# Optimization experiments

Hardware: AMD Instinct MI355X
Metric: run time of the kernel (lower is better)

The kernel has to match this reference:

```python
import jax, jax.numpy as jnp
import numpy as np

N_QUBITS = 8
N_LAYERS = 2


def _ry(theta):
    # theta: scalar or (B,) -> (...,2,2) complex64 RY matrix
    c = jnp.cos(theta * 0.5)
    s = jnp.sin(theta * 0.5)
    return jnp.stack([jnp.stack([c, -s], -1), jnp.stack([s, c], -1)], -2).astype(jnp.complex64)


def _rz(theta):
    # theta: scalar -> (2,2) complex64 RZ matrix diag(e^{-i t/2}, e^{i t/2})
    e = jnp.exp(-0.5j * theta.astype(jnp.complex64))
    z = jnp.zeros_like(e)
    return jnp.stack([jnp.stack([e, z], -1), jnp.stack([z, jnp.conj(e)], -1)], -2)


def _apply_1q(psi, U, wire):
    # U: (2,2) shared across batch; psi: (B, 2,2,...,2)
    ax = wire + 1
    psi = jnp.moveaxis(psi, ax, -1)
    psi = jnp.einsum('...i,ji->...j', psi, U)
    return jnp.moveaxis(psi, -1, ax)


def _apply_1q_batched(psi, U, wire):
    # U: (B,2,2) per-sample gate (angle embedding)
    ax = wire + 1
    psi = jnp.moveaxis(psi, ax, -1)
    psi = jnp.einsum('b...i,bji->b...j', psi, U)
    return jnp.moveaxis(psi, -1, ax)


def _apply_cnot(psi, ctrl, tgt):
    c_ax, t_ax = ctrl + 1, tgt + 1
    psi0 = jnp.take(psi, 0, axis=c_ax)
    psi1 = jnp.take(psi, 1, axis=c_ax)
    t2 = t_ax - 1 if t_ax > c_ax else t_ax
    psi1 = jnp.flip(psi1, axis=t2)  # X on target when control=1
    return jnp.stack([psi0, psi1], axis=c_ax)


def _circuit(x, weights):
    n = N_QUBITS
    B = x.shape[0]
    psi = jnp.zeros((B,) + (2,) * n, jnp.complex64)
    psi = psi.at[(slice(None),) + (0,) * n].set(1.0)
    ang = x * (np.pi / 2)
    for layer in range(weights.shape[0]):
        # AngleEmbedding: RY(x_i * pi/2) on each wire, per-sample angles
        for i in range(n):
            psi = _apply_1q_batched(psi, _ry(ang[:, i]), i)
        # trainable rotations
        for i in range(n):
            psi = _apply_1q(psi, _ry(weights[layer, i, 0]), i)
            psi = _apply_1q(psi, _rz(weights[layer, i, 1]), i)
        # CNOT ring
        for i in range(n - 1):
            psi = _apply_cnot(psi, i, i + 1)
        psi = _apply_cnot(psi, n - 1, 0)
    # <Z_i> = sum_s |psi_s|^2 * (+1 if bit_i(s)==0 else -1)
    p = (psi.real ** 2 + psi.imag ** 2).reshape(B, 2 ** n)
    bits = (jnp.arange(2 ** n)[:, None] >> (n - 1 - jnp.arange(n))) & 1
    zsign = (1 - 2 * bits).astype(jnp.float32)  # (256, 8)
    return (p @ zsign).astype(jnp.float32)


def setup_inputs() -> dict:
    key = jax.random.key(0)
    k1, k2 = jax.random.split(key)
    x = jax.random.uniform(k1, (65536, N_QUBITS), jnp.float32)
    weights = jax.random.uniform(k2, (N_LAYERS, N_QUBITS, 2), jnp.float32) * (2.0 * np.pi)
    return {"x": x, "weights": weights}


def reference(x, weights):
    return _circuit(x, weights)
```

## Files before the change

kernel.cpp:

```cpp
#include <hip/hip_runtime.h>

#define PI_OVER_2 1.57079632679489661923f


__global__ __launch_bounds__(256) void qpauli2_kernel(
        const float* __restrict__ x, const float* __restrict__ w,
        float* __restrict__ out, int nsamples) {
    const int sample = blockIdx.x * blockDim.x + threadIdx.x;
    if (sample >= nsamples) return;

    const float4* xv = reinterpret_cast<const float4*>(x + (size_t)sample * 8);
    const float4 xa = xv[0], xb = xv[1];
    const float xs[8] = {xa.x, xa.y, xa.z, xa.w, xb.x, xb.y, xb.z, xb.w};

    float C[8], S[8], zb[8], xbv[8], yb[8];
#pragma unroll
    for (int q = 0; q < 8; ++q) {
        const float A1 = fmaf(xs[q], PI_OVER_2, w[2 * q]);
        const float W  = w[2 * q + 1];
        const float A2 = fmaf(xs[q], PI_OVER_2, w[16 + 2 * q]);
        float s1v, c1v, sw, cw;
        __sincosf(A1, &s1v, &c1v);
        __sincosf(W, &sw, &cw);
        __sincosf(A2, &S[q], &C[q]);
        zb[q] = c1v;
        xbv[q] = s1v * cw;
        yb[q] = s1v * sw;
    }
    float ZT[9];
    ZT[8] = 1.f;
#pragma unroll
    for (int k = 7; k >= 2; --k) ZT[k] = zb[k] * ZT[k + 1];

    float o[8];

    float fre[16], fim[16];
#pragma unroll
    for (int i2 = 0; i2 < 16; ++i2) { fre[i2] = 0.f; fim[i2] = 0.f; }
    fre[2] = C[0];
    fre[6] = C[0] * zb[0];
    fre[1] = -S[0] * xbv[0];
    fim[5] = S[0] * yb[0];

#define FSTEP(Q)                                                              \
    {                                                                         \
        const float Cz = C[Q] * zb[Q], Cx = C[Q] * xbv[Q], Cy = C[Q] * yb[Q]; \
        const float Sz = S[Q] * zb[Q], Sx = S[Q] * xbv[Q], Sy = S[Q] * yb[Q]; \
        float nre[16], nim[16];                                               \
        _Pragma("unroll")                                                     \
        for (int i2 = 0; i2 < 16; ++i2) { nre[i2] = 0.f; nim[i2] = 0.f; }     \
        _Pragma("unroll")                                                     \
        for (int st = 0; st < 16; ++st) {                                     \
            const int dp_ = st & 1, z0 = (st >> 1) & 1;                       \
            const int H = (st >> 2) & 1, P = (st >> 3) & 1;                   \
            _Pragma("unroll")                                                 \
            for (int d = 0; d < 2; ++d) {                                     \
                const int mx = dp_ ^ d;                                       \
                const int mz = z0 ^ H ^ P;                                    \
                const int ns = d | (z0 << 1) | (H << 2) | ((P ^ d ^ 1) << 3); \
                if (mx == 0 && mz == 0) {                                     \
                    const float F = d ? -S[Q] : C[Q];                         \
                    nre[ns] = fmaf(F, fre[st], nre[ns]);                      \
                    nim[ns] = fmaf(F, fim[st], nim[ns]);                      \
                } else if (mx == 0 && mz == 1) {                              \
                    const float F = d ? -Sz : Cz;                             \
                    nre[ns] = fmaf(F, fre[st], nre[ns]);                      \
                    nim[ns] = fmaf(F, fim[st], nim[ns]);                      \
                } else if (mx == 1 && mz == 0) {                              \
                    const float F = d ? -Sx : Cx;                             \
                    nre[ns] = fmaf(F, fre[st], nre[ns]);                      \
                    nim[ns] = fmaf(F, fim[st], nim[ns]);                      \
                } else {                \
                    const float F = d ? -Sy : Cy;                             \
                    nre[ns] = fmaf(F, fim[st], nre[ns]);                      \
                    nim[ns] = fmaf(-F, fre[st], nim[ns]);                     \
                }                                                             \
            }                                                                 \
        }                                                                     \
        _Pragma("unroll")                                                     \
        for (int i2 = 0; i2 < 16; ++i2) { fre[i2] = nre[i2]; fim[i2] = nim[i2]; } \
    }

#define FCLOSE(I)                                                             \
    {                                                                         \
        const float tz = ZT[(I) + 1];                    \
        const float ty = yb[(I) + 1] * ZT[(I) + 2];                           \
        const float tx = xbv[(I) + 1];                                        \
        float acc = 0.f;                                                      \
        _Pragma("unroll")                                                     \
        for (int st = 0; st < 16; ++st) {                                     \
            const int dp_ = st & 1, z0 = (st >> 1) & 1;                       \
            const int H = (st >> 2) & 1, P = (st >> 3) & 1;                   \
            if (H == P) {                                                     \
                if (dp_ == 0 && z0 == 0)      acc += fre[st];                 \
                else if (dp_ == 0 && z0 == 1) acc = fmaf(fre[st], tz, acc);   \
                else if (dp_ == 1 && z0 == 0) acc = fmaf(fre[st], tx, acc);   \
                else                          acc = fmaf(fim[st], ty, acc);   \
            }                                                                 \
        }                                                                     \
        o[I] = acc;                                                           \
    }

    FSTEP(1) FCLOSE(1)
    FSTEP(2) FCLOSE(2)
    FSTEP(3) FCLOSE(3)
    FSTEP(4) FCLOSE(4)
    FSTEP(5) FCLOSE(5)
    FSTEP(6) FCLOSE(6)
#undef FSTEP
#undef FCLOSE

    float bre[16], bim[16];
#pragma unroll
    for (int i2 = 0; i2 < 16; ++i2) { bre[i2] = 0.f; bim[i2] = 0.f; }
    bre[2] = C[7]; bre[6] = C[7];
    bre[9] = -S[7]; bre[13] = -S[7];

#define BSTEP(Q, ISQ0)                                                        \
    {                                                                         \
        const float Cz = C[Q] * zb[(Q) + 1], Cx = C[Q] * xbv[(Q) + 1];        \
        const float Cy = C[Q] * yb[(Q) + 1];                                  \
        const float Sz = S[Q] * zb[(Q) + 1], Sx = S[Q] * xbv[(Q) + 1];        \
        const float Sy = S[Q] * yb[(Q) + 1];                                  \
        float nre[16], nim[16];                                               \
        _Pragma("unroll")                                                     \
        for (int i2 = 0; i2 < 16; ++i2) { nre[i2] = 0.f; nim[i2] = 0.f; }     \
        _Pragma("unroll")                                                     \
        for (int st = 0; st < 16; ++st) {                                     \
            const int dp_ = st & 1, s1 = (st >> 1) & 1;                       \
            const int g = (st >> 2) & 1, dt = (st >> 3) & 1;                  \
            _Pragma("unroll")                                                 \
            for (int dl = 0; dl < 2; ++dl) {                                  \
                const int mx = dl ^ dp_ ^ ((ISQ0) ? dt : 0);                  \
                const int mz = g ^ s1;                                        \
                const int ns = dl | ((s1 ^ 1 ^ dl) << 1) | (g << 2) | (dt << 3); \
                if (mx == 0 && mz == 0) {                                     \
                    const float F = dl ? -S[Q] : C[Q];                        \
                    nre[ns] = fmaf(F, bre[st], nre[ns]);                      \
                    nim[ns] = fmaf(F, bim[st], nim[ns]);                      \
                } else if (mx == 0 && mz == 1) {                              \
                    const float F = dl ? -Sz : Cz;                            \
                    nre[ns] = fmaf(F, bre[st], nre[ns]);                      \
                    nim[ns] = fmaf(F, bim[st], nim[ns]);                      \
                } else if (mx == 1 && mz == 0) {                              \
                    const float F = dl ? -Sx : Cx;                            \
                    nre[ns] = fmaf(F, bre[st], nre[ns]);                      \
                    nim[ns] = fmaf(F, bim[st], nim[ns]);                      \
                } else {                                                      \
                    const float F = dl ? -Sy : Cy;                            \
                    nre[ns] = fmaf(F, bim[st], nre[ns]);                      \
                    nim[ns] = fmaf(-F, bre[st], nim[ns]);                     \
                }                                                             \
            }                                                                 \
        }                                                                     \
        _Pragma("unroll")                                                     \
        for (int i2 = 0; i2 < 16; ++i2) { bre[i2] = nre[i2]; bim[i2] = nim[i2]; } \
    }

    BSTEP(6, 0)
    BSTEP(5, 0)
    BSTEP(4, 0)
    BSTEP(3, 0)
    BSTEP(2, 0)
    BSTEP(1, 0)

#define APPLYG(MX, MZ, J)                                                     \
    if ((MX) == 0 && (MZ) == 1) { r *= zb[J]; i *= zb[J]; }                   \
    else if ((MX) == 1 && (MZ) == 0) { r *= xbv[J]; i *= xbv[J]; }            \
    else if ((MX) == 1 && (MZ) == 1) {                                        \
        const float t = r; r = i * yb[J]; i = -t * yb[J]; }

    {
        float acc = 0.f;
#pragma unroll
        for (int st = 0; st < 16; ++st) {
            const int dp_ = st & 1, sf = (st >> 1) & 1;
            const int g = (st >> 2) & 1, dt = (st >> 3) & 1;
            if (g) continue;
            float r = bre[st], i = bim[st];
            APPLYG(dt, sf, 0)
            APPLYG(dp_ ^ dt, sf, 1)
            acc += r;
        }
        o[0] = acc;
    }

    BSTEP(0, 1)
    {
        float acc = 0.f;
#pragma unroll
        for (int st = 0; st < 16; ++st) {
            const int dp_ = st & 1, sf = (st >> 1) & 1;
            const int g = (st >> 2) & 1, dt = (st >> 3) & 1;
            if (g != (1 ^ dp_)) continue;
            float r = bre[st], i = bim[st];
            APPLYG(dp_ ^ dt, sf ^ g, 0)
            acc += r;
        }
        o[7] = acc;
    }
#undef APPLYG
#undef BSTEP

    float4* ov = reinterpret_cast<float4*>(out + (size_t)sample * 8);
    ov[0] = make_float4(o[0], o[1], o[2], o[3]);
    ov[1] = make_float4(o[4], o[5], o[6], o[7]);
}

extern "C" void kernel_launch(void* const* d_in, const int* in_sizes, int n_in,
                              void* d_out, int out_size, void* d_ws, size_t ws_size,
                              hipStream_t stream) {
    const float* x = (const float*)d_in[0];
    const float* w = (const float*)d_in[1];
    float* outp = (float*)d_out;
    const int nsamples = in_sizes[0] / 8;
    const int block = 256;
    const int grid = (nsamples + block - 1) / block;
    qpauli2_kernel<<<grid, block, 0, stream>>>(x, w, outp, nsamples);
}
```

Measured before the change: 10.56 us.

## Split forward and backward passes across paired wavefronts per sample

Each sample is now handled by two wavefronts. One runs the forward chain that produces outputs 1-6, the other runs the backward chain that produces outputs 0 and 7. The split is done at wave granularity, so neither wave diverges. The ping-pong buffers replace the per-step temporaries and copy-back, which lowers register pressure. Outputs become scalar stores instead of float4. The cost is duplicated input loads and sincos work, and twice as many threads.

```diff
diff --git a/kernel.cpp b/kernel.cpp
--- a/kernel.cpp
+++ b/kernel.cpp
@@ -3,10 +3,13 @@
 #define PI_OVER_2 1.57079632679489661923f
 
 
-__global__ __launch_bounds__(256) void qpauli2_kernel(
+__global__ __launch_bounds__(256) void qpauli3_kernel(
         const float* __restrict__ x, const float* __restrict__ w,
         float* __restrict__ out, int nsamples) {
-    const int sample = blockIdx.x * blockDim.x + threadIdx.x;
+    const int gid = blockIdx.x * blockDim.x + threadIdx.x;
+    const int wave = gid >> 6, lane = gid & 63;
+    const int which = wave & 1;
+    const int sample = (wave >> 1) * 64 + lane;
     if (sample >= nsamples) return;
 
     const float4* xv = reinterpret_cast<const float4*>(x + (size_t)sample * 8);
@@ -27,28 +30,30 @@
         xbv[q] = s1v * cw;
         yb[q] = s1v * sw;
     }
-    float ZT[9];
-    ZT[8] = 1.f;
-#pragma unroll
-    for (int k = 7; k >= 2; --k) ZT[k] = zb[k] * ZT[k + 1];
-
-    float o[8];
-
-    float fre[16], fim[16];
-#pragma unroll
-    for (int i2 = 0; i2 < 16; ++i2) { fre[i2] = 0.f; fim[i2] = 0.f; }
-    fre[2] = C[0];
-    fre[6] = C[0] * zb[0];
-    fre[1] = -S[0] * xbv[0];
-    fim[5] = S[0] * yb[0];
-
-#define FSTEP(Q)                                                              \
+
+    float* o = out + (size_t)sample * 8;
+
+    float Are[16], Aim[16], Bre[16], Bim[16];
+#pragma unroll
+    for (int i2 = 0; i2 < 16; ++i2) { Are[i2] = 0.f; Aim[i2] = 0.f; }
+
+    if (which == 0) {
+        float ZT[9];
+        ZT[8] = 1.f;
+#pragma unroll
+        for (int k = 7; k >= 2; --k) ZT[k] = zb[k] * ZT[k + 1];
+
+        Are[2] = C[0];
+        Are[6] = C[0] * zb[0];
+        Are[1] = -S[0] * xbv[0];
+        Aim[5] = S[0] * yb[0];
+
+#define FSTEP(Q, IRE, IIM, ORE, OIM)                                          \
     {                                                                         \
         const float Cz = C[Q] * zb[Q], Cx = C[Q] * xbv[Q], Cy = C[Q] * yb[Q]; \
         const float Sz = S[Q] * zb[Q], Sx = S[Q] * xbv[Q], Sy = S[Q] * yb[Q]; \
-        float nre[16], nim[16];                                               \
-        _Pragma("unroll")                                                     \
-        for (int i2 = 0; i2 < 16; ++i2) { nre[i2] = 0.f; nim[i2] = 0.f; }     \
+        _Pragma("unroll")                                                     \
+        for (int i2 = 0; i2 < 16; ++i2) { ORE[i2] = 0.f; OIM[i2] = 0.f; }     \
         _Pragma("unroll")                                                     \
         for (int st = 0; st < 16; ++st) {                                     \
             const int dp_ = st & 1, z0 = (st >> 1) & 1;                       \
@@ -60,30 +65,28 @@
                 const int ns = d | (z0 << 1) | (H << 2) | ((P ^ d ^ 1) << 3); \
                 if (mx == 0 && mz == 0) {                                     \
                     const float F = d ? -S[Q] : C[Q];                         \
-                    nre[ns] = fmaf(F, fre[st], nre[ns]);                      \
-                    nim[ns] = fmaf(F, fim[st], nim[ns]);                      \
+                    ORE[ns] = fmaf(F, IRE[st], ORE[ns]);                      \
+                    OIM[ns] = fmaf(F, IIM[st], OIM[ns]);                      \
                 } else if (mx == 0 && mz == 1) {                              \
                     const float F = d ? -Sz : Cz;                             \
-                    nre[ns] = fmaf(F, fre[st], nre[ns]);                      \
-                    nim[ns] = fmaf(F, fim[st], nim[ns]);                      \
+                    ORE[ns] = fmaf(F, IRE[st], ORE[ns]);                      \
+                    OIM[ns] = fmaf(F, IIM[st], OIM[ns]);                      \
                 } else if (mx == 1 && mz == 0) {                              \
                     const float F = d ? -Sx : Cx;                             \
-                    nre[ns] = fmaf(F, fre[st], nre[ns]);                      \
-                    nim[ns] = fmaf(F, fim[st], nim[ns]);                      \
-                } else {                \
+                    ORE[ns] = fmaf(F, IRE[st], ORE[ns]);                      \
+                    OIM[ns] = fmaf(F, IIM[st], OIM[ns]);                      \
+                } else {                                          \
                     const float F = d ? -Sy : Cy;                             \
-                    nre[ns] = fmaf(F, fim[st], nre[ns]);                      \
-                    nim[ns] = fmaf(-F, fre[st], nim[ns]);                     \
+                    ORE[ns] = fmaf(F, IIM[st], ORE[ns]);                      \
+                    OIM[ns] = fmaf(-F, IRE[st], OIM[ns]);                     \
                 }                                                             \
             }                                                                 \
         }                                                                     \
-        _Pragma("unroll")                                                     \
-        for (int i2 = 0; i2 < 16; ++i2) { fre[i2] = nre[i2]; fim[i2] = nim[i2]; } \
-    }
-
-#define FCLOSE(I)                                                             \
+    }
+
+#define FCLOSE(I, RRE, RIM)                                                   \
     {                                                                         \
-        const float tz = ZT[(I) + 1];                    \
+        const float tz = ZT[(I) + 1];                                         \
         const float ty = yb[(I) + 1] * ZT[(I) + 2];                           \
         const float tx = xbv[(I) + 1];                                        \
         float acc = 0.f;                                                      \
@@ -92,39 +95,35 @@
             const int dp_ = st & 1, z0 = (st >> 1) & 1;                       \
             const int H = (st >> 2) & 1, P = (st >> 3) & 1;                   \
             if (H == P) {                                                     \
-                if (dp_ == 0 && z0 == 0)      acc += fre[st];                 \
-                else if (dp_ == 0 && z0 == 1) acc = fmaf(fre[st], tz, acc);   \
-                else if (dp_ == 1 && z0 == 0) acc = fmaf(fre[st], tx, acc);   \
-                else                          acc = fmaf(fim[st], ty, acc);   \
+                if (dp_ == 0 && z0 == 0)      acc += RRE[st];                 \
+                else if (dp_ == 0 && z0 == 1) acc = fmaf(RRE[st], tz, acc);   \
+                else if (dp_ == 1 && z0 == 0) acc = fmaf(RRE[st], tx, acc);   \
+                else                          acc = fmaf(RIM[st], ty, acc);   \
             }                                                                 \
         }                                                                     \
         o[I] = acc;                                                           \
     }
 
-    FSTEP(1) FCLOSE(1)
-    FSTEP(2) FCLOSE(2)
-    FSTEP(3) FCLOSE(3)
-    FSTEP(4) FCLOSE(4)
-    FSTEP(5) FCLOSE(5)
-    FSTEP(6) FCLOSE(6)
+        FSTEP(1, Are, Aim, Bre, Bim) FCLOSE(1, Bre, Bim)
+        FSTEP(2, Bre, Bim, Are, Aim) FCLOSE(2, Are, Aim)
+        FSTEP(3, Are, Aim, Bre, Bim) FCLOSE(3, Bre, Bim)
+        FSTEP(4, Bre, Bim, Are, Aim) FCLOSE(4, Are, Aim)
+        FSTEP(5, Are, Aim, Bre, Bim) FCLOSE(5, Bre, Bim)
+        FSTEP(6, Bre, Bim, Are, Aim) FCLOSE(6, Are, Aim)
 #undef FSTEP
 #undef FCLOSE
-
-    float bre[16], bim[16];
-#pragma unroll
-    for (int i2 = 0; i2 < 16; ++i2) { bre[i2] = 0.f; bim[i2] = 0.f; }
-    bre[2] = C[7]; bre[6] = C[7];
-    bre[9] = -S[7]; bre[13] = -S[7];
-
-#define BSTEP(Q, ISQ0)                                                        \
+    } else {
+        Are[2] = C[7]; Are[6] = C[7];
+        Are[9] = -S[7]; Are[13] = -S[7];
+
+#define BSTEP(Q, ISQ0, IRE, IIM, ORE, OIM)                                    \
     {                                                                         \
         const float Cz = C[Q] * zb[(Q) + 1], Cx = C[Q] * xbv[(Q) + 1];        \
         const float Cy = C[Q] * yb[(Q) + 1];                                  \
         const float Sz = S[Q] * zb[(Q) + 1], Sx = S[Q] * xbv[(Q) + 1];        \
         const float Sy = S[Q] * yb[(Q) + 1];                                  \
-        float nre[16], nim[16];                                               \
-        _Pragma("unroll")                                                     \
-        for (int i2 = 0; i2 < 16; ++i2) { nre[i2] = 0.f; nim[i2] = 0.f; }     \
+        _Pragma("unroll")                                                     \
+        for (int i2 = 0; i2 < 16; ++i2) { ORE[i2] = 0.f; OIM[i2] = 0.f; }     \
         _Pragma("unroll")                                                     \
         for (int st = 0; st < 16; ++st) {                                     \
             const int dp_ = st & 1, s1 = (st >> 1) & 1;                       \
@@ -136,33 +135,31 @@
                 const int ns = dl | ((s1 ^ 1 ^ dl) << 1) | (g << 2) | (dt << 3); \
                 if (mx == 0 && mz == 0) {                                     \
                     const float F = dl ? -S[Q] : C[Q];                        \
-                    nre[ns] = fmaf(F, bre[st], nre[ns]);                      \
-                    nim[ns] = fmaf(F, bim[st], nim[ns]);                      \
+                    ORE[ns] = fmaf(F, IRE[st], ORE[ns]);                      \
+                    OIM[ns] = fmaf(F, IIM[st], OIM[ns]);                      \
                 } else if (mx == 0 && mz == 1) {                              \
                     const float F = dl ? -Sz : Cz;                            \
-                    nre[ns] = fmaf(F, bre[st], nre[ns]);                      \
-                    nim[ns] = fmaf(F, bim[st], nim[ns]);                      \
+                    ORE[ns] = fmaf(F, IRE[st], ORE[ns]);                      \
+                    OIM[ns] = fmaf(F, IIM[st], OIM[ns]);                      \
                 } else if (mx == 1 && mz == 0) {                              \
                     const float F = dl ? -Sx : Cx;                            \
-                    nre[ns] = fmaf(F, bre[st], nre[ns]);                      \
-                    nim[ns] = fmaf(F, bim[st], nim[ns]);                      \
+                    ORE[ns] = fmaf(F, IRE[st], ORE[ns]);                      \
+                    OIM[ns] = fmaf(F, IIM[st], OIM[ns]);                      \
                 } else {                                                      \
                     const float F = dl ? -Sy : Cy;                            \
-                    nre[ns] = fmaf(F, bim[st], nre[ns]);                      \
-                    nim[ns] = fmaf(-F, bre[st], nim[ns]);                     \
+                    ORE[ns] = fmaf(F, IIM[st], ORE[ns]);                      \
+                    OIM[ns] = fmaf(-F, IRE[st], OIM[ns]);                     \
                 }                                                             \
             }                                                                 \
         }                                                                     \
-        _Pragma("unroll")                                                     \
-        for (int i2 = 0; i2 < 16; ++i2) { bre[i2] = nre[i2]; bim[i2] = nim[i2]; } \
-    }
-
-    BSTEP(6, 0)
-    BSTEP(5, 0)
-    BSTEP(4, 0)
-    BSTEP(3, 0)
-    BSTEP(2, 0)
-    BSTEP(1, 0)
+    }
+
+        BSTEP(6, 0, Are, Aim, Bre, Bim)
+        BSTEP(5, 0, Bre, Bim, Are, Aim)
+        BSTEP(4, 0, Are, Aim, Bre, Bim)
+        BSTEP(3, 0, Bre, Bim, Are, Aim)
+        BSTEP(2, 0, Are, Aim, Bre, Bim)
+        BSTEP(1, 0, Bre, Bim, Are, Aim)
 
 #define APPLYG(MX, MZ, J)                                                     \
     if ((MX) == 0 && (MZ) == 1) { r *= zb[J]; i *= zb[J]; }                   \
@@ -170,41 +167,38 @@
     else if ((MX) == 1 && (MZ) == 1) {                                        \
         const float t = r; r = i * yb[J]; i = -t * yb[J]; }
 
-    {
-        float acc = 0.f;
-#pragma unroll
-        for (int st = 0; st < 16; ++st) {
-            const int dp_ = st & 1, sf = (st >> 1) & 1;
-            const int g = (st >> 2) & 1, dt = (st >> 3) & 1;
-            if (g) continue;
-            float r = bre[st], i = bim[st];
-            APPLYG(dt, sf, 0)
-            APPLYG(dp_ ^ dt, sf, 1)
-            acc += r;
+        {
+            float acc = 0.f;
+#pragma unroll
+            for (int st = 0; st < 16; ++st) {
+                const int dp_ = st & 1, sf = (st >> 1) & 1;
+                const int g = (st >> 2) & 1, dt = (st >> 3) & 1;
+                if (g) continue;
+                float r = Are[st], i = Aim[st];
+                APPLYG(dt, sf, 0)
+                APPLYG(dp_ ^ dt, sf, 1)
+                acc += r;
+            }
+            o[0] = acc;
         }
-        o[0] = acc;
-    }
-
-    BSTEP(0, 1)
-    {
-        float acc = 0.f;
-#pragma unroll
-        for (int st = 0; st < 16; ++st) {
-            const int dp_ = st & 1, sf = (st >> 1) & 1;
-            const int g = (st >> 2) & 1, dt = (st >> 3) & 1;
-            if (g != (1 ^ dp_)) continue;
-            float r = bre[st], i = bim[st];
-            APPLYG(dp_ ^ dt, sf ^ g, 0)
-            acc += r;
+
+        BSTEP(0, 1, Are, Aim, Bre, Bim)
+        {
+            float acc = 0.f;
+#pragma unroll
+            for (int st = 0; st < 16; ++st) {
+                const int dp_ = st & 1, sf = (st >> 1) & 1;
+                const int g = (st >> 2) & 1, dt = (st >> 3) & 1;
+                if (g != (1 ^ dp_)) continue;
+                float r = Bre[st], i = Bim[st];
+                APPLYG(dp_ ^ dt, sf ^ g, 0)
+                acc += r;
+            }
+            o[7] = acc;
         }
-        o[7] = acc;
-    }
 #undef APPLYG
 #undef BSTEP
-
-    float4* ov = reinterpret_cast<float4*>(out + (size_t)sample * 8);
-    ov[0] = make_float4(o[0], o[1], o[2], o[3]);
-    ov[1] = make_float4(o[4], o[5], o[6], o[7]);
+    }
 }
 
 extern "C" void kernel_launch(void* const* d_in, const int* in_sizes, int n_in,
@@ -214,7 +208,8 @@
     const float* w = (const float*)d_in[1];
     float* outp = (float*)d_out;
     const int nsamples = in_sizes[0] / 8;
+    const int nthreads = nsamples * 2;
     const int block = 256;
-    const int grid = (nsamples + block - 1) / block;
-    qpauli2_kernel<<<grid, block, 0, stream>>>(x, w, outp, nsamples);
+    const int grid = (nthreads + block - 1) / block;
+    qpauli3_kernel<<<grid, block, 0, stream>>>(x, w, outp, nsamples);
 }
```

Measured after the change: 9.912 us. 1.07x faster.
